# Optimization experiments

Measured on AMD Instinct MI355X. Metric: run time of the kernel, lower is better.

The kernel has to match this reference:

```python
import jax, jax.numpy as jnp
import numpy as np

NLAYER = 3
EPS = 1e-5
NEG = -1e30  # stand-in for -inf in masked max


def _layernorm(h, g, b):
    mu = h.mean(-1, keepdims=True)
    v = ((h - mu) ** 2).mean(-1, keepdims=True)
    return (h - mu) * jax.lax.rsqrt(v + EPS) * g + b


def setup_inputs() -> dict:
    key = jax.random.key(0)
    ks = jax.random.split(key, 8)
    N, K, D = 8192, 8, 128
    s = 0.05
    x = jax.random.normal(ks[0], (N, D), jnp.float32)
    neigh = jax.random.randint(ks[1], (N, K), 0, N, dtype=jnp.int32)
    nbr_count = jax.random.randint(ks[2], (N,), 0, K + 1, dtype=jnp.int32)
    gcn_W = jax.random.normal(ks[3], (NLAYER, D, D), jnp.float32) * s
    gcn_b = jnp.zeros((NLAYER, D), jnp.float32)
    gcn_ln_g = jnp.ones((NLAYER, D), jnp.float32)
    gcn_ln_b = jnp.zeros((NLAYER, D), jnp.float32)
    sage_pool_W = jax.random.normal(ks[4], (D, D), jnp.float32) * s
    sage_pool_b = jnp.zeros((D,), jnp.float32)
    sage_merge_W = jax.random.normal(ks[5], (NLAYER, D, 2 * D), jnp.float32) * s
    sage_merge_b = jnp.zeros((NLAYER, D), jnp.float32)
    sage_ln_g = jnp.ones((NLAYER - 1, D), jnp.float32)
    sage_ln_b = jnp.zeros((NLAYER - 1, D), jnp.float32)
    return {"x": x, "neigh": neigh, "nbr_count": nbr_count,
            "gcn_W": gcn_W, "gcn_b": gcn_b, "gcn_ln_g": gcn_ln_g, "gcn_ln_b": gcn_ln_b,
            "sage_pool_W": sage_pool_W, "sage_pool_b": sage_pool_b,
            "sage_merge_W": sage_merge_W, "sage_merge_b": sage_merge_b,
            "sage_ln_g": sage_ln_g, "sage_ln_b": sage_ln_b}


def reference(x, neigh, nbr_count, gcn_W, gcn_b, gcn_ln_g, gcn_ln_b,
              sage_pool_W, sage_pool_b, sage_merge_W, sage_merge_b,
              sage_ln_g, sage_ln_b):
    N, D = x.shape
    K = neigh.shape[1]
    mask = jnp.arange(K)[None, :] < nbr_count[:, None]  # [N, K] valid neighbors

    # ---- GCN branch: dense symmetric-normalized adjacency with self loops ----
    rows = jnp.broadcast_to(jnp.arange(N)[:, None], neigh.shape)
    A = jnp.zeros((N, N), x.dtype).at[rows, neigh].add(mask.astype(x.dtype))
    A = jnp.minimum(A, 1.0)  # dedupe multi-edges (original sets 1.0)
    A = A.at[jnp.arange(N), jnp.arange(N)].set(1.0)  # self loop (node[0] in list)
    dinv = jax.lax.rsqrt(A.sum(-1))  # degree^-0.5, >= 1 due to self loop
    Ah = dinv[:, None] * A * dinv[None, :]

    h = x
    first = None
    for i in range(NLAYER):
        nxt = h @ gcn_W[i].T + gcn_b[i]
        if i == 0:
            first = nxt
        nxt = jax.nn.relu(Ah @ nxt)
        # residual=True: layer 1 adds first-layer pre-prop enc, later layers add h
        h = _layernorm(nxt + (first if i == 0 else h), gcn_ln_g[i], gcn_ln_b[i])
    gcn_out = h

    # ---- SAGE branch: max-pool over children (self excluded), concat, merge ----
    def pool(node_encs):
        g = jnp.where(mask[:, :, None], node_encs[neigh], NEG)  # [N, K, D]
        p = g.max(axis=1)
        return jnp.where((nbr_count > 0)[:, None], p, 0.0)  # leaf -> zeros

    ne1 = jax.nn.relu(x @ sage_pool_W.T + sage_pool_b)  # pool linear only layer 1
    s = jax.nn.relu(jnp.concatenate([x, pool(ne1)], -1) @ sage_merge_W[0].T + sage_merge_b[0])
    for i in range(1, NLAYER):
        nxt = jax.nn.relu(jnp.concatenate([s, pool(s)], -1) @ sage_merge_W[i].T + sage_merge_b[i])
        s = _layernorm(nxt + s, sage_ln_g[i - 1], sage_ln_b[i - 1])

    return jnp.concatenate([gcn_out, s], -1)  # [N, 2*treehid]
```

## Files before the change

### kernel.cpp

```cpp
#include <hip/hip_runtime.h>

#define NND 8192
#define KNBR 8
#define DD 128
#define EPSF 1e-5f
#define TSH 16384

typedef __attribute__((ext_vector_type(8))) short bf16x8;
typedef __attribute__((ext_vector_type(4))) float f32x4;

__device__ __forceinline__ unsigned short f2bf(float f) {
    unsigned u = __float_as_uint(f);
    u += 0x7FFF + ((u >> 16) & 1);
    return (unsigned short)(u >> 16);
}

__device__ __forceinline__ float bf_lo(unsigned u) { return __uint_as_float(u << 16); }
__device__ __forceinline__ float bf_hi(unsigned u) { return __uint_as_float(u & 0xFFFF0000u); }

__device__ __forceinline__ bf16x8 cvt8(const float* __restrict__ p) {
    float4 lo = *(const float4*)p;
    float4 hi = *(const float4*)(p + 4);
    bf16x8 r;
    r[0] = f2bf(lo.x); r[1] = f2bf(lo.y); r[2] = f2bf(lo.z); r[3] = f2bf(lo.w);
    r[4] = f2bf(hi.x); r[5] = f2bf(hi.y); r[6] = f2bf(hi.z); r[7] = f2bf(hi.w);
    return r;
}

__device__ __forceinline__ void gload_lds16(const unsigned short* g, unsigned short* l) {
    __builtin_amdgcn_global_load_lds(
        (const __attribute__((address_space(1))) unsigned int*)(g),
        (__attribute__((address_space(3))) unsigned int*)(l), 16, 0, 0);
}

__device__ __forceinline__ void stage1(unsigned short* sh, const unsigned short* wb, int tid) {
    int lane = tid & 63, w = tid >> 6;
#pragma unroll
    for (int r = 0; r < 8; ++r) {
        int blk = (r * 4 + w) * 512;
        gload_lds16(wb + blk + lane * 8, sh + blk);
    }
}

__device__ __forceinline__ void stage_cvt_sw(unsigned short* sh, const float* __restrict__ W,
                                             int wstr, int tid) {
    int r = tid >> 1, h = tid & 1;
    const float* src = W + (size_t)r * wstr;
#pragma unroll
    for (int i = 0; i < 8; ++i) {
        int ch = h * 8 + i;
        *(bf16x8*)(sh + r * 128 + ((ch ^ (r & 7)) << 3)) = cvt8(src + ch * 8);
    }
}

__device__ __forceinline__ void load_af(bf16x8* af, const unsigned short* __restrict__ A,
                                        int rowBase, int lane) {
    int idx = lane & 15, q = lane >> 4;
    const unsigned short* Ar = A + (size_t)(rowBase + idx) * DD;
#pragma unroll
    for (int s = 0; s < 4; ++s) af[s] = *(const bf16x8*)(Ar + s * 32 + q * 8);
}

__device__ __forceinline__ void load_af_f32(bf16x8* af, const float* __restrict__ A,
                                            int rowBase, int lane) {
    int idx = lane & 15, q = lane >> 4;
    const float* Ar = A + (size_t)(rowBase + idx) * DD;
#pragma unroll
    for (int s = 0; s < 4; ++s) af[s] = cvt8(Ar + s * 32 + q * 8);
}

__device__ __forceinline__ void mma_sw(const bf16x8* af, const unsigned short* shB,
                                       int lane, f32x4* acc) {
    int idx = lane & 15, q = lane >> 4, k7 = idx & 7;
#pragma unroll
    for (int s = 0; s < 4; ++s)
#pragma unroll
        for (int ct = 0; ct < 8; ++ct) {
            int ch = (4 * s + q) ^ k7;
            bf16x8 bf = *(const bf16x8*)(shB + (ct * 16 + idx) * 128 + ch * 8);
            acc[ct] = __builtin_amdgcn_mfma_f32_16x16x32_bf16(af[s], bf, acc[ct], 0, 0, 0);
        }
}

__device__ __forceinline__ void store_fw(float* __restrict__ out, int ostride, int oOff,
        int rowBase, int lane, const f32x4* acc, const float* __restrict__ bias, bool relu) {
    int idx = lane & 15, q = lane >> 4;
#pragma unroll
    for (int ct = 0; ct < 8; ++ct) {
        float b = bias[ct * 16 + idx];
#pragma unroll
        for (int r = 0; r < 4; ++r) {
            float v = acc[ct][r] + b;
            if (relu) v = fmaxf(v, 0.f);
            out[(size_t)(rowBase + q * 4 + r) * ostride + oOff + ct * 16 + idx] = v;
        }
    }
}

__device__ __forceinline__ void store_fw_b16(unsigned short* __restrict__ out,
        int rowBase, int lane, const f32x4* acc, const float* __restrict__ bias, bool relu) {
    int idx = lane & 15, q = lane >> 4;
#pragma unroll
    for (int ct = 0; ct < 8; ++ct) {
        float b = bias[ct * 16 + idx];
#pragma unroll
        for (int r = 0; r < 4; ++r) {
            float v = acc[ct][r] + b;
            if (relu) v = fmaxf(v, 0.f);
            out[(size_t)(rowBase + q * 4 + r) * DD + ct * 16 + idx] = f2bf(v);
        }
    }
}

__device__ __forceinline__ void lnstore_fw(float* __restrict__ out, int ostride, int oOff,
        const float* __restrict__ resid, int rowBase, int lane, f32x4* acc,
        const float* __restrict__ bias, const float* __restrict__ g,
        const float* __restrict__ bv, unsigned short* __restrict__ outB) {
    int idx = lane & 15, q = lane >> 4;
    float rsum[4] = {0.f, 0.f, 0.f, 0.f};
#pragma unroll
    for (int ct = 0; ct < 8; ++ct) {
        float b = bias[ct * 16 + idx];
#pragma unroll
        for (int r = 0; r < 4; ++r) {
            float t = fmaxf(acc[ct][r] + b, 0.f)
                    + resid[(size_t)(rowBase + q * 4 + r) * DD + ct * 16 + idx];
            acc[ct][r] = t;
            rsum[r] += t;
        }
    }
#pragma unroll
    for (int r = 0; r < 4; ++r)
#pragma unroll
        for (int m = 1; m < 16; m <<= 1) rsum[r] += __shfl_xor(rsum[r], m, 64);
    float mu[4];
#pragma unroll
    for (int r = 0; r < 4; ++r) mu[r] = rsum[r] * (1.f / 128.f);
    float var[4] = {0.f, 0.f, 0.f, 0.f};
#pragma unroll
    for (int ct = 0; ct < 8; ++ct)
#pragma unroll
        for (int r = 0; r < 4; ++r) {
            float d = acc[ct][r] - mu[r];
            var[r] += d * d;
        }
#pragma unroll
    for (int r = 0; r < 4; ++r)
#pragma unroll
        for (int m = 1; m < 16; m <<= 1) var[r] += __shfl_xor(var[r], m, 64);
    float rs[4];
#pragma unroll
    for (int r = 0; r < 4; ++r) rs[r] = rsqrtf(var[r] * (1.f / 128.f) + EPSF);
#pragma unroll
    for (int ct = 0; ct < 8; ++ct) {
        float gg = g[ct * 16 + idx], bb = bv[ct * 16 + idx];
#pragma unroll
        for (int r = 0; r < 4; ++r) {
            float o = (acc[ct][r] - mu[r]) * rs[r] * gg + bb;
            size_t row = (size_t)(rowBase + q * 4 + r);
            out[row * ostride + oOff + ct * 16 + idx] = o;
            if (outB) outB[row * DD + ct * 16 + idx] = f2bf(o);
        }
    }
}

__device__ __forceinline__ float wave_sum(float s) {
#pragma unroll
    for (int m = 1; m < 64; m <<= 1) s += __shfl_xor(s, m, 64);
    return s;
}

__device__ __forceinline__ void prop_ln_row_b(int row, int lane,
        const unsigned short* __restrict__ nxtB, const unsigned short* __restrict__ residB,
        const float* __restrict__ dinv, const int* __restrict__ kept,
        const int* __restrict__ neigh,
        const float* __restrict__ g, const float* __restrict__ b,
        float* __restrict__ outF, int oStride, int oOff,
        unsigned short* __restrict__ outB) {
    const unsigned* nxt2 = (const unsigned*)nxtB;
    float di = dinv[row];
    int km = kept[row];
    int idxs[KNBR]; float wj[KNBR];
#pragma unroll
    for (int j = 0; j < KNBR; ++j) {
        int nb = neigh[row * KNBR + j];
        bool k = (km >> j) & 1;
        idxs[j] = k ? nb : row;
        wj[j] = k ? dinv[nb] : 0.f;
    }
    unsigned vv[KNBR];
#pragma unroll
    for (int j = 0; j < KNBR; ++j) vv[j] = nxt2[(size_t)idxs[j] * 64 + lane];
    unsigned su = nxt2[(size_t)row * 64 + lane];
    float ax = di * bf_lo(su), ay = di * bf_hi(su);
#pragma unroll
    for (int j = 0; j < KNBR; ++j) {
        ax = fmaf(wj[j], bf_lo(vv[j]), ax);
        ay = fmaf(wj[j], bf_hi(vv[j]), ay);
    }
    unsigned ru = ((const unsigned*)residB)[(size_t)row * 64 + lane];
    float vx = fmaxf(di * ax, 0.f) + bf_lo(ru);
    float vy = fmaxf(di * ay, 0.f) + bf_hi(ru);
    float mu = wave_sum(vx + vy) * (1.f / 128.f);
    float dx = vx - mu, dy = vy - mu;
    float var = wave_sum(dx * dx + dy * dy) * (1.f / 128.f);
    float rs = rsqrtf(var + EPSF);
    float2 gg = ((const float2*)g)[lane];
    float2 bb = ((const float2*)b)[lane];
    float ox = dx * rs * gg.x + bb.x;
    float oy = dy * rs * gg.y + bb.y;
    if (outF) {
        float2 o; o.x = ox; o.y = oy;
        *reinterpret_cast<float2*>(outF + (size_t)row * oStride + oOff + lane * 2) = o;
    }
    if (outB) {
        unsigned pk = (unsigned)f2bf(ox) | ((unsigned)f2bf(oy) << 16);
        *(unsigned*)(outB + (size_t)row * DD + lane * 2) = pk;
    }
}

__device__ __forceinline__ void pool_row_b(int row, int lane,
        const unsigned short* __restrict__ enc, const int* __restrict__ neigh,
        const int* __restrict__ cnt, unsigned short* __restrict__ P) {
    int c = cnt[row];
    const unsigned* e32 = (const unsigned*)enc;
    unsigned vv[KNBR];
#pragma unroll
    for (int j = 0; j < KNBR; ++j) {
        int nb = neigh[row * KNBR + j];
        int src = (j < c) ? nb : row;
        vv[j] = e32[(size_t)src * 64 + lane];
    }
    float ax = -1e30f, ay = -1e30f;
#pragma unroll
    for (int j = 0; j < KNBR; ++j) {
        if (j < c) {
            ax = fmaxf(ax, bf_lo(vv[j]));
            ay = fmaxf(ay, bf_hi(vv[j]));
        }
    }
    unsigned o = 0u;
    if (c > 0)
        o = (__float_as_uint(ax) >> 16) | (__float_as_uint(ay) & 0xFFFF0000u);
    ((unsigned*)P)[(size_t)row * 64 + lane] = o;
}

__global__ __launch_bounds__(256)
void mega_all(const float* __restrict__ x,
              const float* __restrict__ gcnW, const float* __restrict__ poolW,
              const float* __restrict__ mW,
              const float* __restrict__ gB0, const float* __restrict__ pB,
              const float* __restrict__ mB0,
              const int* __restrict__ neigh, const int* __restrict__ cnt,
              float* __restrict__ dinv, int* __restrict__ kept,
              unsigned short* __restrict__ wbuf,
              unsigned short* __restrict__ Gb, unsigned short* __restrict__ E1b,
              float* __restrict__ S1) {
    __shared__ __align__(16) unsigned short shB[TSH];
    const int bid = blockIdx.x, tid = threadIdx.x;
    const int lane = tid & 63, w = tid >> 6;

    if (bid < 384) {
        int grp = bid >> 7, bx = bid & 127;
        const float* W; int str;
        if (grp == 0)      { W = gcnW;  str = 128; }
        else if (grp == 1) { W = poolW; str = 128; }
        else               { W = mW;    str = 256; }
        stage_cvt_sw(shB, W, str, tid);
        int rowBase = (bx * 4 + w) * 16;
        bf16x8 af[4];
        load_af_f32(af, x, rowBase, lane);
        __syncthreads();
        f32x4 acc[8];
#pragma unroll
        for (int i = 0; i < 8; ++i) acc[i] = (f32x4){0.f, 0.f, 0.f, 0.f};
        mma_sw(af, shB, lane, acc);
        if (grp == 0)      store_fw_b16(Gb, rowBase, lane, acc, gB0, false);
        else if (grp == 1) store_fw_b16(E1b, rowBase, lane, acc, pB, true);
        else               store_fw(S1, DD, 0, rowBase, lane, acc, mB0, false);
    } else if (bid < 416) {
        int i = (bid - 384) * 256 + tid;
        int c = cnt[i];
        int nb[KNBR];
#pragma unroll
        for (int j = 0; j < KNBR; ++j) nb[j] = neigh[i * KNBR + j];
        int mask = 0, deg = 1;
#pragma unroll
        for (int j = 0; j < KNBR; ++j) {
            if (j < c) {
                int v = nb[j];
                bool dup = (v == i);
                for (int jj = 0; jj < j; ++jj)
                    if (nb[jj] == v) { dup = true; }
                if (!dup) { mask |= (1 << j); deg++; }
            }
        }
        dinv[i] = rsqrtf((float)deg);
        kept[i] = mask;
    } else {
        int cid = (bid - 416) * 256 + tid;
        int u = cid >> 11, c2 = cid & 2047, row = c2 >> 4, ch = c2 & 15;
        const float* base; int str; int t;
        if (u == 0)      { t = 1; base = gcnW + 16384;       str = 128; }
        else if (u == 1) { t = 2; base = gcnW + 32768;       str = 128; }
        else if (u == 2) { t = 5; base = mW + 128;           str = 256; }
        else if (u == 3) { t = 6; base = mW + 32768;         str = 256; }
        else if (u == 4) { t = 7; base = mW + 32768 + 128;   str = 256; }
        else if (u == 5) { t = 8; base = mW + 65536;         str = 256; }
        else             { t = 9; base = mW + 65536 + 128;   str = 256; }
        bf16x8 v = cvt8(base + (size_t)row * str + ch * 8);
        *(bf16x8*)(wbuf + t * TSH + row * 128 + ((ch ^ (row & 7)) << 3)) = v;
    }
}

__global__ __launch_bounds__(256)
void prop_pool(const unsigned short* __restrict__ nxtB,
               const unsigned short* __restrict__ residB,
               const float* __restrict__ dinv, const int* __restrict__ kept,
               const int* __restrict__ neigh, const int* __restrict__ cnt,
               const float* __restrict__ g, const float* __restrict__ b,
               float* __restrict__ outF, int oStride,
               unsigned short* __restrict__ outB,
               const unsigned short* __restrict__ enc,
               unsigned short* __restrict__ P) {
    int row = blockIdx.x * 4 + (threadIdx.x >> 6);
    int lane = threadIdx.x & 63;
    prop_ln_row_b(row, lane, nxtB, residB, dinv, kept, neigh, g, b,
                  outF, oStride, 0, outB);
    pool_row_b(row, lane, enc, neigh, cnt, P);
}

__global__ __launch_bounds__(256)
void gemm_step4(const unsigned short* __restrict__ Pb, const unsigned short* __restrict__ H1b,
                const unsigned short* __restrict__ wbuf, const float* __restrict__ gB1,
                float* __restrict__ S, unsigned short* __restrict__ S1b,
                unsigned short* __restrict__ Gb) {
    __shared__ __align__(16) unsigned short shB[TSH];
    const int tid = threadIdx.x, lane = tid & 63, w = tid >> 6;
    const int rowBase = ((int)blockIdx.x * 4 + w) * 16;
    f32x4 acc[8];
#pragma unroll
    for (int i = 0; i < 8; ++i) acc[i] = (f32x4){0.f, 0.f, 0.f, 0.f};
    bf16x8 af[4];
    if (blockIdx.y == 0) {
        stage1(shB, wbuf + 5 * TSH, tid);
        load_af(af, Pb, rowBase, lane);
        __syncthreads();
        mma_sw(af, shB, lane, acc);
        int idx = lane & 15, q = lane >> 4;
#pragma unroll
        for (int ct = 0; ct < 8; ++ct)
#pragma unroll
            for (int r = 0; r < 4; ++r) {
                size_t o = (size_t)(rowBase + q * 4 + r) * DD + ct * 16 + idx;
                float v = fmaxf(S[o] + acc[ct][r], 0.f);
                S[o] = v;
                S1b[o] = f2bf(v);
            }
    } else {
        stage1(shB, wbuf + 1 * TSH, tid);
        load_af(af, H1b, rowBase, lane);
        __syncthreads();
        mma_sw(af, shB, lane, acc);
        store_fw_b16(Gb, rowBase, lane, acc, gB1, false);
    }
}

__global__ __launch_bounds__(256)
void gemm_step6(const unsigned short* __restrict__ S1b, const unsigned short* __restrict__ Pb,
                const unsigned short* __restrict__ H2b, const float* __restrict__ S1,
                const unsigned short* __restrict__ wbuf,
                const float* __restrict__ mB1, const float* __restrict__ gB2,
                const float* __restrict__ sg, const float* __restrict__ sb,
                float* __restrict__ S2, unsigned short* __restrict__ S2b,
                unsigned short* __restrict__ Gb) {
    __shared__ __align__(16) unsigned short shB[2 * TSH];
    const int tid = threadIdx.x, lane = tid & 63, w = tid >> 6;
    const int rowBase = ((int)blockIdx.x * 4 + w) * 16;
    f32x4 acc[8];
#pragma unroll
    for (int i = 0; i < 8; ++i) acc[i] = (f32x4){0.f, 0.f, 0.f, 0.f};
    if (blockIdx.y == 0) {
        stage1(shB, wbuf + 6 * TSH, tid);
        stage1(shB + TSH, wbuf + 7 * TSH, tid);
        bf16x8 af1[4], af2[4];
        load_af(af1, S1b, rowBase, lane);
        load_af(af2, Pb, rowBase, lane);
        __syncthreads();
        mma_sw(af1, shB, lane, acc);
        mma_sw(af2, shB + TSH, lane, acc);
        lnstore_fw(S2, DD, 0, S1, rowBase, lane, acc, mB1, sg, sb, S2b);
    } else {
        stage1(shB, wbuf + 2 * TSH, tid);
        bf16x8 af[4];
        load_af(af, H2b, rowBase, lane);
        __syncthreads();
        mma_sw(af, shB, lane, acc);
        store_fw_b16(Gb, rowBase, lane, acc, gB2, false);
    }
}

__global__ __launch_bounds__(256)
void gemm_final(const unsigned short* __restrict__ S2b, const unsigned short* __restrict__ Pb,
                const float* __restrict__ S2, const unsigned short* __restrict__ wbuf,
                const float* __restrict__ mB2,
                const float* __restrict__ sg2, const float* __restrict__ sb2,
                float* __restrict__ out) {
    __shared__ __align__(16) unsigned short shB[2 * TSH];
    const int tid = threadIdx.x, lane = tid & 63, w = tid >> 6;
    const int rowBase = ((int)blockIdx.x * 4 + w) * 16;
    f32x4 acc[8];
#pragma unroll
    for (int i = 0; i < 8; ++i) acc[i] = (f32x4){0.f, 0.f, 0.f, 0.f};
    stage1(shB, wbuf + 8 * TSH, tid);
    stage1(shB + TSH, wbuf + 9 * TSH, tid);
    bf16x8 af1[4], af2[4];
    load_af(af1, S2b, rowBase, lane);
    load_af(af2, Pb, rowBase, lane);
    __syncthreads();
    mma_sw(af1, shB, lane, acc);
    mma_sw(af2, shB + TSH, lane, acc);
    lnstore_fw(out, 2 * DD, DD, S2, rowBase, lane, acc, mB2, sg2, sb2, nullptr);
}

extern "C" void kernel_launch(void* const* d_in, const int* in_sizes, int n_in,
                              void* d_out, int out_size, void* d_ws, size_t ws_size,
                              hipStream_t stream) {
    (void)in_sizes; (void)n_in; (void)out_size; (void)ws_size;
    const float* x      = (const float*)d_in[0];
    const int*   neigh  = (const int*)d_in[1];
    const int*   cnt    = (const int*)d_in[2];
    const float* gcnW   = (const float*)d_in[3];
    const float* gcnB   = (const float*)d_in[4];
    const float* gcnG   = (const float*)d_in[5];
    const float* gcnBb  = (const float*)d_in[6];
    const float* poolW  = (const float*)d_in[7];
    const float* poolB  = (const float*)d_in[8];
    const float* mW     = (const float*)d_in[9];
    const float* mB     = (const float*)d_in[10];
    const float* sg     = (const float*)d_in[11];
    const float* sb     = (const float*)d_in[12];
    float* out = (float*)d_out;

    char* ws = (char*)d_ws;
    float* dinv = (float*)ws;
    int*   kept = (int*)(ws + 32 * 1024);
    unsigned short* wbuf = (unsigned short*)(ws + 64 * 1024);
    float* S1 = (float*)(ws + 448 * 1024);
    float* S2 = S1 + NND * DD;
    unsigned short* Gb  = (unsigned short*)(S2 + NND * DD);
    unsigned short* E1b = Gb  + NND * DD;
    unsigned short* Pb  = E1b + NND * DD;
    unsigned short* H1b = Pb  + NND * DD;
    unsigned short* H2b = H1b + NND * DD;
    unsigned short* S1b = H2b + NND * DD;
    unsigned short* S2b = S1b + NND * DD;

    dim3 blk(256);
    dim3 rgrid(NND / 4);

    mega_all<<<dim3(472), blk, 0, stream>>>(x, gcnW, poolW, mW, gcnB, poolB, mB,
                                            neigh, cnt, dinv, kept, wbuf,
                                            Gb, E1b, S1);
    prop_pool<<<rgrid, blk, 0, stream>>>(Gb, Gb, dinv, kept, neigh, cnt,
                                         gcnG, gcnBb, nullptr, DD, H1b, E1b, Pb);
    gemm_step4<<<dim3(128, 2), blk, 0, stream>>>(Pb, H1b, wbuf, gcnB + DD,
                                                 S1, S1b, Gb);
    prop_pool<<<rgrid, blk, 0, stream>>>(Gb, H1b, dinv, kept, neigh, cnt,
                                         gcnG + DD, gcnBb + DD, nullptr, DD,
                                         H2b, S1b, Pb);
    gemm_step6<<<dim3(128, 2), blk, 0, stream>>>(S1b, Pb, H2b, S1, wbuf,
                                                 mB + DD, gcnB + 2 * DD, sg, sb,
                                                 S2, S2b, Gb);
    prop_pool<<<rgrid, blk, 0, stream>>>(Gb, H2b, dinv, kept, neigh, cnt,
                                         gcnG + 2 * DD, gcnBb + 2 * DD,
                                         out, 2 * DD, nullptr, S2b, Pb);
    gemm_final<<<dim3(128), blk, 0, stream>>>(S2b, Pb, S2, wbuf, mB + 2 * DD,
                                              sg + DD, sb + DD, out);
}
```

Measured before the change: 141.0 us.

## Split mega kernel into convert pass and bf16 GEMM, drop fp32 SAGE intermediates

The old fused first kernel, which converted weights inside each GEMM block, is split into two launches. A convert/degree kernel pre-converts all weight tiles and x to bf16 once, and a second kernel runs the three input GEMMs from the staged bf16 tiles via async LDS loads. The fp32 SAGE state buffers S1/S2 are replaced by bf16 copies for residuals, cutting global memory traffic. This adds one extra launch and lowers the residual path to bf16 precision, which may slightly change accuracy.

```diff
diff --git a/kernel.cpp b/kernel.cpp
--- a/kernel.cpp
+++ b/kernel.cpp
@@ -17,6 +17,9 @@
 
 __device__ __forceinline__ float bf_lo(unsigned u) { return __uint_as_float(u << 16); }
 __device__ __forceinline__ float bf_hi(unsigned u) { return __uint_as_float(u & 0xFFFF0000u); }
+__device__ __forceinline__ float bfs(unsigned short u) {
+    return __uint_as_float((unsigned)u << 16);
+}
 
 __device__ __forceinline__ bf16x8 cvt8(const float* __restrict__ p) {
     float4 lo = *(const float4*)p;
@@ -42,17 +45,6 @@
     }
 }
 
-__device__ __forceinline__ void stage_cvt_sw(unsigned short* sh, const float* __restrict__ W,
-                                             int wstr, int tid) {
-    int r = tid >> 1, h = tid & 1;
-    const float* src = W + (size_t)r * wstr;
-#pragma unroll
-    for (int i = 0; i < 8; ++i) {
-        int ch = h * 8 + i;
-        *(bf16x8*)(sh + r * 128 + ((ch ^ (r & 7)) << 3)) = cvt8(src + ch * 8);
-    }
-}
-
 __device__ __forceinline__ void load_af(bf16x8* af, const unsigned short* __restrict__ A,
                                         int rowBase, int lane) {
     int idx = lane & 15, q = lane >> 4;
@@ -61,14 +53,6 @@
     for (int s = 0; s < 4; ++s) af[s] = *(const bf16x8*)(Ar + s * 32 + q * 8);
 }
 
-__device__ __forceinline__ void load_af_f32(bf16x8* af, const float* __restrict__ A,
-                                            int rowBase, int lane) {
-    int idx = lane & 15, q = lane >> 4;
-    const float* Ar = A + (size_t)(rowBase + idx) * DD;
-#pragma unroll
-    for (int s = 0; s < 4; ++s) af[s] = cvt8(Ar + s * 32 + q * 8);
-}
-
 __device__ __forceinline__ void mma_sw(const bf16x8* af, const unsigned short* shB,
                                        int lane, f32x4* acc) {
     int idx = lane & 15, q = lane >> 4, k7 = idx & 7;
@@ -82,21 +66,6 @@
         }
 }
 
-__device__ __forceinline__ void store_fw(float* __restrict__ out, int ostride, int oOff,
-        int rowBase, int lane, const f32x4* acc, const float* __restrict__ bias, bool relu) {
-    int idx = lane & 15, q = lane >> 4;
-#pragma unroll
-    for (int ct = 0; ct < 8; ++ct) {
-        float b = bias[ct * 16 + idx];
-#pragma unroll
-        for (int r = 0; r < 4; ++r) {
-            float v = acc[ct][r] + b;
-            if (relu) v = fmaxf(v, 0.f);
-            out[(size_t)(rowBase + q * 4 + r) * ostride + oOff + ct * 16 + idx] = v;
-        }
-    }
-}
-
 __device__ __forceinline__ void store_fw_b16(unsigned short* __restrict__ out,
         int rowBase, int lane, const f32x4* acc, const float* __restrict__ bias, bool relu) {
     int idx = lane & 15, q = lane >> 4;
@@ -112,8 +81,8 @@
     }
 }
 
-__device__ __forceinline__ void lnstore_fw(float* __restrict__ out, int ostride, int oOff,
-        const float* __restrict__ resid, int rowBase, int lane, f32x4* acc,
+__device__ __forceinline__ void lnstore_fw_br(float* __restrict__ outF, int ostride, int oOff,
+        const unsigned short* __restrict__ residB, int rowBase, int lane, f32x4* acc,
         const float* __restrict__ bias, const float* __restrict__ g,
         const float* __restrict__ bv, unsigned short* __restrict__ outB) {
     int idx = lane & 15, q = lane >> 4;
@@ -124,7 +93,7 @@
 #pragma unroll
         for (int r = 0; r < 4; ++r) {
             float t = fmaxf(acc[ct][r] + b, 0.f)
-                    + resid[(size_t)(rowBase + q * 4 + r) * DD + ct * 16 + idx];
+                    + bfs(residB[(size_t)(rowBase + q * 4 + r) * DD + ct * 16 + idx]);
             acc[ct][r] = t;
             rsum[r] += t;
         }
@@ -158,7 +127,7 @@
         for (int r = 0; r < 4; ++r) {
             float o = (acc[ct][r] - mu[r]) * rs[r] * gg + bb;
             size_t row = (size_t)(rowBase + q * 4 + r);
-            out[row * ostride + oOff + ct * 16 + idx] = o;
+            if (outF) outF[row * ostride + oOff + ct * 16 + idx] = o;
             if (outB) outB[row * DD + ct * 16 + idx] = f2bf(o);
         }
     }
@@ -246,40 +215,14 @@
 }
 
 __global__ __launch_bounds__(256)
-void mega_all(const float* __restrict__ x,
-              const float* __restrict__ gcnW, const float* __restrict__ poolW,
-              const float* __restrict__ mW,
-              const float* __restrict__ gB0, const float* __restrict__ pB,
-              const float* __restrict__ mB0,
-              const int* __restrict__ neigh, const int* __restrict__ cnt,
-              float* __restrict__ dinv, int* __restrict__ kept,
-              unsigned short* __restrict__ wbuf,
-              unsigned short* __restrict__ Gb, unsigned short* __restrict__ E1b,
-              float* __restrict__ S1) {
-    __shared__ __align__(16) unsigned short shB[TSH];
-    const int bid = blockIdx.x, tid = threadIdx.x;
-    const int lane = tid & 63, w = tid >> 6;
-
-    if (bid < 384) {
-        int grp = bid >> 7, bx = bid & 127;
-        const float* W; int str;
-        if (grp == 0)      { W = gcnW;  str = 128; }
-        else if (grp == 1) { W = poolW; str = 128; }
-        else               { W = mW;    str = 256; }
-        stage_cvt_sw(shB, W, str, tid);
-        int rowBase = (bx * 4 + w) * 16;
-        bf16x8 af[4];
-        load_af_f32(af, x, rowBase, lane);
-        __syncthreads();
-        f32x4 acc[8];
-#pragma unroll
-        for (int i = 0; i < 8; ++i) acc[i] = (f32x4){0.f, 0.f, 0.f, 0.f};
-        mma_sw(af, shB, lane, acc);
-        if (grp == 0)      store_fw_b16(Gb, rowBase, lane, acc, gB0, false);
-        else if (grp == 1) store_fw_b16(E1b, rowBase, lane, acc, pB, true);
-        else               store_fw(S1, DD, 0, rowBase, lane, acc, mB0, false);
-    } else if (bid < 416) {
-        int i = (bid - 384) * 256 + tid;
+void cvt_deg(const int* __restrict__ neigh, const int* __restrict__ cnt,
+             const float* __restrict__ gcnW, const float* __restrict__ poolW,
+             const float* __restrict__ mW, const float* __restrict__ x,
+             float* __restrict__ dinv, int* __restrict__ kept,
+             unsigned short* __restrict__ wbuf, unsigned short* __restrict__ xb) {
+    int bx = blockIdx.x, tid = threadIdx.x;
+    if (bx < 32) {
+        int i = bx * 256 + tid;
         int c = cnt[i];
         int nb[KNBR];
 #pragma unroll
@@ -297,20 +240,44 @@
         }
         dinv[i] = rsqrtf((float)deg);
         kept[i] = mask;
-    } else {
-        int cid = (bid - 416) * 256 + tid;
-        int u = cid >> 11, c2 = cid & 2047, row = c2 >> 4, ch = c2 & 15;
-        const float* base; int str; int t;
-        if (u == 0)      { t = 1; base = gcnW + 16384;       str = 128; }
-        else if (u == 1) { t = 2; base = gcnW + 32768;       str = 128; }
-        else if (u == 2) { t = 5; base = mW + 128;           str = 256; }
-        else if (u == 3) { t = 6; base = mW + 32768;         str = 256; }
-        else if (u == 4) { t = 7; base = mW + 32768 + 128;   str = 256; }
-        else if (u == 5) { t = 8; base = mW + 65536;         str = 256; }
-        else             { t = 9; base = mW + 65536 + 128;   str = 256; }
+    } else if (bx < 112) {
+        int cid = (bx - 32) * 256 + tid;
+        int t = cid >> 11, c2 = cid & 2047, row = c2 >> 4, ch = c2 & 15;
+        const float* base; int str;
+        if (t < 3)       { base = gcnW + t * 16384; str = 128; }
+        else if (t == 3) { base = poolW; str = 128; }
+        else { int u = t - 4; base = mW + (u >> 1) * 32768 + (u & 1) * 128; str = 256; }
         bf16x8 v = cvt8(base + (size_t)row * str + ch * 8);
         *(bf16x8*)(wbuf + t * TSH + row * 128 + ((ch ^ (row & 7)) << 3)) = v;
-    }
+    } else {
+        int i = (bx - 112) * 256 + tid;
+        *(bf16x8*)(xb + (size_t)i * 8) = cvt8(x + (size_t)i * 8);
+    }
+}
+
+__global__ __launch_bounds__(256)
+void mega_gemm(const unsigned short* __restrict__ xb,
+               const unsigned short* __restrict__ wbuf,
+               const float* __restrict__ gB0, const float* __restrict__ pB,
+               const float* __restrict__ mB0,
+               unsigned short* __restrict__ Gb, unsigned short* __restrict__ E1b,
+               unsigned short* __restrict__ S1pb) {
+    __shared__ __align__(16) unsigned short shB[TSH];
+    const int tid = threadIdx.x, lane = tid & 63, w = tid >> 6;
+    const int grp = blockIdx.y;
+    const int tile = (grp == 0) ? 0 : (grp == 1) ? 3 : 4;
+    stage1(shB, wbuf + tile * TSH, tid);
+    const int rowBase = ((int)blockIdx.x * 4 + w) * 16;
+    bf16x8 af[4];
+    load_af(af, xb, rowBase, lane);
+    __syncthreads();
+    f32x4 acc[8];
+#pragma unroll
+    for (int i = 0; i < 8; ++i) acc[i] = (f32x4){0.f, 0.f, 0.f, 0.f};
+    mma_sw(af, shB, lane, acc);
+    if (grp == 0)      store_fw_b16(Gb, rowBase, lane, acc, gB0, false);
+    else if (grp == 1) store_fw_b16(E1b, rowBase, lane, acc, pB, true);
+    else               store_fw_b16(S1pb, rowBase, lane, acc, mB0, false);
 }
 
 __global__ __launch_bounds__(256)
@@ -333,7 +300,7 @@
 __global__ __launch_bounds__(256)
 void gemm_step4(const unsigned short* __restrict__ Pb, const unsigned short* __restrict__ H1b,
                 const unsigned short* __restrict__ wbuf, const float* __restrict__ gB1,
-                float* __restrict__ S, unsigned short* __restrict__ S1b,
+                const unsigned short* __restrict__ S1pb, unsigned short* __restrict__ S1b,
                 unsigned short* __restrict__ Gb) {
     __shared__ __align__(16) unsigned short shB[TSH];
     const int tid = threadIdx.x, lane = tid & 63, w = tid >> 6;
@@ -353,8 +320,7 @@
 #pragma unroll
             for (int r = 0; r < 4; ++r) {
                 size_t o = (size_t)(rowBase + q * 4 + r) * DD + ct * 16 + idx;
-                float v = fmaxf(S[o] + acc[ct][r], 0.f);
-                S[o] = v;
+                float v = fmaxf(bfs(S1pb[o]) + acc[ct][r], 0.f);
                 S1b[o] = f2bf(v);
             }
     } else {
@@ -368,12 +334,11 @@
 
 __global__ __launch_bounds__(256)
 void gemm_step6(const unsigned short* __restrict__ S1b, const unsigned short* __restrict__ Pb,
-                const unsigned short* __restrict__ H2b, const float* __restrict__ S1,
+                const unsigned short* __restrict__ H2b,
                 const unsigned short* __restrict__ wbuf,
                 const float* __restrict__ mB1, const float* __restrict__ gB2,
                 const float* __restrict__ sg, const float* __restrict__ sb,
-                float* __restrict__ S2, unsigned short* __restrict__ S2b,
-                unsigned short* __restrict__ Gb) {
+                unsigned short* __restrict__ S2b, unsigned short* __restrict__ Gb) {
     __shared__ __align__(16) unsigned short shB[2 * TSH];
     const int tid = threadIdx.x, lane = tid & 63, w = tid >> 6;
     const int rowBase = ((int)blockIdx.x * 4 + w) * 16;
@@ -389,7 +354,7 @@
         __syncthreads();
         mma_sw(af1, shB, lane, acc);
         mma_sw(af2, shB + TSH, lane, acc);
-        lnstore_fw(S2, DD, 0, S1, rowBase, lane, acc, mB1, sg, sb, S2b);
+        lnstore_fw_br(nullptr, DD, 0, S1b, rowBase, lane, acc, mB1, sg, sb, S2b);
     } else {
         stage1(shB, wbuf + 2 * TSH, tid);
         bf16x8 af[4];
@@ -402,7 +367,7 @@
 
 __global__ __launch_bounds__(256)
 void gemm_final(const unsigned short* __restrict__ S2b, const unsigned short* __restrict__ Pb,
-                const float* __restrict__ S2, const unsigned short* __restrict__ wbuf,
+                const unsigned short* __restrict__ wbuf,
                 const float* __restrict__ mB2,
                 const float* __restrict__ sg2, const float* __restrict__ sb2,
                 float* __restrict__ out) {
@@ -420,7 +385,7 @@
     __syncthreads();
     mma_sw(af1, shB, lane, acc);
     mma_sw(af2, shB + TSH, lane, acc);
-    lnstore_fw(out, 2 * DD, DD, S2, rowBase, lane, acc, mB2, sg2, sb2, nullptr);
+    lnstore_fw_br(out, 2 * DD, DD, S2b, rowBase, lane, acc, mB2, sg2, sb2, nullptr);
 }
 
 extern "C" void kernel_launch(void* const* d_in, const int* in_sizes, int n_in,
@@ -446,35 +411,36 @@
     float* dinv = (float*)ws;
     int*   kept = (int*)(ws + 32 * 1024);
     unsigned short* wbuf = (unsigned short*)(ws + 64 * 1024);
-    float* S1 = (float*)(ws + 448 * 1024);
-    float* S2 = S1 + NND * DD;
-    unsigned short* Gb  = (unsigned short*)(S2 + NND * DD);
-    unsigned short* E1b = Gb  + NND * DD;
-    unsigned short* Pb  = E1b + NND * DD;
-    unsigned short* H1b = Pb  + NND * DD;
-    unsigned short* H2b = H1b + NND * DD;
-    unsigned short* S1b = H2b + NND * DD;
-    unsigned short* S2b = S1b + NND * DD;
+    unsigned short* xb   = (unsigned short*)(ws + 448 * 1024);
+    unsigned short* Gb   = xb   + NND * DD;
+    unsigned short* E1b  = Gb   + NND * DD;
+    unsigned short* S1pb = E1b  + NND * DD;
+    unsigned short* Pb   = S1pb + NND * DD;
+    unsigned short* H1b  = Pb   + NND * DD;
+    unsigned short* H2b  = H1b  + NND * DD;
+    unsigned short* S1b  = H2b  + NND * DD;
+    unsigned short* S2b  = S1b  + NND * DD;
 
     dim3 blk(256);
     dim3 rgrid(NND / 4);
 
-    mega_all<<<dim3(472), blk, 0, stream>>>(x, gcnW, poolW, mW, gcnB, poolB, mB,
-                                            neigh, cnt, dinv, kept, wbuf,
-                                            Gb, E1b, S1);
+    cvt_deg<<<dim3(624), blk, 0, stream>>>(neigh, cnt, gcnW, poolW, mW, x,
+                                           dinv, kept, wbuf, xb);
+    mega_gemm<<<dim3(128, 3), blk, 0, stream>>>(xb, wbuf, gcnB, poolB, mB,
+                                                Gb, E1b, S1pb);
     prop_pool<<<rgrid, blk, 0, stream>>>(Gb, Gb, dinv, kept, neigh, cnt,
                                          gcnG, gcnBb, nullptr, DD, H1b, E1b, Pb);
     gemm_step4<<<dim3(128, 2), blk, 0, stream>>>(Pb, H1b, wbuf, gcnB + DD,
-                                                 S1, S1b, Gb);
+                                                 S1pb, S1b, Gb);
     prop_pool<<<rgrid, blk, 0, stream>>>(Gb, H1b, dinv, kept, neigh, cnt,
                                          gcnG + DD, gcnBb + DD, nullptr, DD,
                                          H2b, S1b, Pb);
-    gemm_step6<<<dim3(128, 2), blk, 0, stream>>>(S1b, Pb, H2b, S1, wbuf,
+    gemm_step6<<<dim3(128, 2), blk, 0, stream>>>(S1b, Pb, H2b, wbuf,
                                                  mB + DD, gcnB + 2 * DD, sg, sb,
-                                                 S2, S2b, Gb);
+                                                 S2b, Gb);
     prop_pool<<<rgrid, blk, 0, stream>>>(Gb, H2b, dinv, kept, neigh, cnt,
                                          gcnG + 2 * DD, gcnBb + 2 * DD,
                                          out, 2 * DD, nullptr, S2b, Pb);
-    gemm_final<<<dim3(128), blk, 0, stream>>>(S2b, Pb, S2, wbuf, mB + 2 * DD,
+    gemm_final<<<dim3(128), blk, 0, stream>>>(S2b, Pb, wbuf, mB + 2 * DD,
                                               sg + DD, sb + DD, out);
 }
```

New measurement: 131.9 us. -6.4%, faster.
